# Performance work log

Hardware: AMD Instinct MI355X
Metric: run time of the kernel (lower is better)

Reference implementation:

```python
import jax, jax.numpy as jnp
import numpy as np

CHUNK = 128
KERNEL_EPS = 1e-4
ATTN_EPS = 1e-6


def _gaussian_orthogonal_random_matrix(nb_rows, nb_cols, seed=0):
    # scaling=0: rows of stacked orthogonal blocks, scaled by chi-distributed norms
    rng = np.random.default_rng(seed)
    blocks = []
    n_full = nb_rows // nb_cols
    for _ in range(n_full):
        qm, _ = np.linalg.qr(rng.standard_normal((nb_cols, nb_cols)))
        blocks.append(qm.T)
    rem = nb_rows - n_full * nb_cols
    if rem > 0:
        qm, _ = np.linalg.qr(rng.standard_normal((nb_cols, nb_cols)))
        blocks.append(qm.T[:rem])
    mat = np.concatenate(blocks, axis=0)
    multiplier = np.linalg.norm(rng.standard_normal((nb_rows, nb_cols)), axis=1)
    return (multiplier[:, None] * mat).astype(np.float32)


def softmax_kernel(data, proj, is_query):
    # data: [b,h,n,d], proj: [m,d]
    d = data.shape[-1]
    m = proj.shape[0]
    data_normalizer = d ** -0.25
    ratio = m ** -0.5
    data_dash = jnp.einsum('bhnd,md->bhnm', data * data_normalizer, proj)
    diag_data = (data ** 2).sum(-1, keepdims=True) * 0.5 * (data_normalizer ** 2)
    if is_query:
        stab = jnp.max(data_dash, axis=-1, keepdims=True)
    else:
        stab = jnp.max(data_dash)
    return ratio * (jnp.exp(data_dash - diag_data - stab) + KERNEL_EPS)


def chunked_causal_linear_attention(qf, kf, v):
    # qf,kf: [b,h,n,m]; v: [b,h,n,e]
    b, h, n, m = qf.shape
    e = v.shape[-1]
    nc = n // CHUNK
    to_chunks = lambda t: t.reshape(b, h, nc, CHUNK, -1).transpose(2, 0, 1, 3, 4)
    qc, kc, vc = to_chunks(qf), to_chunks(kf), to_chunks(v)  # [nc,b,h,c,*]

    def step(carry, xs):
        Z, S = carry  # Z: [b,h,m], S: [b,h,m,e]
        q, k, vv = xs
        k_cum = Z[:, :, None, :] + jnp.cumsum(k, axis=2)          # [b,h,c,m]
        D_inv = 1.0 / jnp.einsum('bhcm,bhcm->bhc', q, k_cum + ATTN_EPS)
        ctx = jnp.einsum('bhcm,bhce->bhcme', k, vv)               # [b,h,c,m,e]
        ctx_cum = S[:, :, None, :, :] + jnp.cumsum(ctx, axis=2)
        out = jnp.einsum('bhcme,bhcm,bhc->bhce', ctx_cum, q, D_inv)
        return (k_cum[:, :, -1, :], ctx_cum[:, :, -1, :, :]), out

    Z0 = jnp.zeros((b, h, m), qf.dtype)
    S0 = jnp.zeros((b, h, m, e), qf.dtype)
    (Z, S), outs = jax.lax.scan(jax.checkpoint(step), (Z0, S0), (qc, kc, vc))
    out = outs.transpose(1, 2, 0, 3, 4).reshape(b, h, n, e)
    return out, Z, S


def setup_inputs() -> dict:
    key = jax.random.key(0)
    kq, kk, kv = jax.random.split(key, 3)
    B, H, N, D, M = 2, 8, 4096, 64, 256
    q = jax.random.normal(kq, (B, H, N, D), dtype=jnp.float32)
    k = jax.random.normal(kk, (B, H, N, D), dtype=jnp.float32)
    v = jax.random.normal(kv, (B, H, N, D), dtype=jnp.float32)
    projection_matrix = jnp.asarray(_gaussian_orthogonal_random_matrix(M, D))
    return {"q": q, "k": k, "v": v, "projection_matrix": projection_matrix,
            "inferrring_states": 1}


def reference(q, k, v, projection_matrix, inferrring_states):
    qf = softmax_kernel(q, projection_matrix, is_query=True)
    kf = softmax_kernel(k, projection_matrix, is_query=False)
    out, Z, S = chunked_causal_linear_attention(qf, kf, v)
    return (out, Z, S)
```

## Files before the change

### kernel.cpp

```cpp
#include <hip/hip_runtime.h>

typedef unsigned short ushort_t;
typedef __attribute__((ext_vector_type(8))) short bf16x8;
typedef __attribute__((ext_vector_type(8))) _Float16 f16x8;
typedef __attribute__((ext_vector_type(16))) float f32x16;

#define NORMC 0.35355339059327373f
#define DIAGC 0.0625f
#define RATIO 0.0625f
#define KEPS  1e-4f
#define AEPS  1e-6f
#define KAPPA (RATIO*KEPS)

__device__ __forceinline__ unsigned short f2bf(float f){
  unsigned u = __float_as_uint(f);
  unsigned r = (u + 0x7FFFu + ((u >> 16) & 1u)) >> 16;
  return (unsigned short)r;
}
__device__ __forceinline__ float bf2f(unsigned short h){
  return __uint_as_float(((unsigned)h) << 16);
}
__device__ __forceinline__ unsigned enc_f(float f){
  unsigned u = __float_as_uint(f);
  return (u & 0x80000000u) ? ~u : (u | 0x80000000u);
}
__device__ __forceinline__ float dec_f(unsigned e){
  unsigned b = (e & 0x80000000u) ? (e ^ 0x80000000u) : ~e;
  return __uint_as_float(b);
}
__device__ __forceinline__ unsigned short h2u(_Float16 h){
  union { _Float16 h; unsigned short u; } c; c.h = h; return c.u;
}
__device__ __forceinline__ unsigned pk2h(float a, float b){
  return (unsigned)h2u((_Float16)a) | ((unsigned)h2u((_Float16)b) << 16);
}

__global__ void k_prep(const float* __restrict__ proj, ushort_t* __restrict__ pjh,
                       unsigned* __restrict__ kmax){
  int t = threadIdx.x;
  if (t == 0) *kmax = 0u;
  for (int d = 0; d < 64; ++d){
    float val = NORMC * proj[t*64 + d];
    pjh[t*64 + d] = h2u((_Float16)val);
  }
}

__launch_bounds__(512, 4)
__global__ void k_featQ(const float* __restrict__ q, const ushort_t* __restrict__ pjh,
                        ushort_t* __restrict__ qf)
{
  extern __shared__ char sm[];
  char* Bp = sm;
  char* Xh = sm + 32768;
  char* Xl = sm + 49152;
  float* dsm = (float*)(sm + 65536);
  float* rmx = (float*)(sm + 66048);

  int tid = threadIdx.x;
  int w   = tid >> 6;
  int wr  = w & 3;
  int wc  = w >> 2;
  int lane= tid & 63;
  int l31 = lane & 31;
  int half= lane >> 5;
  int tile = (int)blockIdx.x;
  int row0 = tile * 128;

  for (int i = tid; i < 2048; i += 512){
    int m = i >> 3, c8 = i & 7;
    int rgn = ((m>>5)*4 + (c8>>1))*2 + (c8&1);
    int slot = (m & 31) ^ ((rgn & 7) << 2);
    *(uint4*)(Bp + rgn*512 + slot*16) = *(const uint4*)(pjh + m*64 + c8*8);
  }
  #pragma unroll
  for (int it = 0; it < 4; ++it){
    int g = it*512 + tid;
    int row = g >> 4, c4 = g & 15;
    float4 xv = *(const float4*)(q + (size_t)(row0+row)*64 + c4*4);
    _Float16 h0=(_Float16)xv.x, h1=(_Float16)xv.y, h2=(_Float16)xv.z, h3=(_Float16)xv.w;
    float l0 = xv.x-(float)h0, l1 = xv.y-(float)h1, l2 = xv.z-(float)h2, l3 = xv.w-(float)h3;
    int rgn = ((row>>5)*4 + (c4>>2))*2 + ((c4>>1)&1);
    int off = rgn*512 + (((row&31) ^ ((c4>>1)<<2)))*16 + (c4&1)*8;
    uint2 ph; ph.x = (unsigned)h2u(h0)|((unsigned)h2u(h1)<<16);
              ph.y = (unsigned)h2u(h2)|((unsigned)h2u(h3)<<16);
    uint2 pl; pl.x = pk2h(l0,l1); pl.y = pk2h(l2,l3);
    *(uint2*)(Xh + off) = ph;
    *(uint2*)(Xl + off) = pl;
    float ssq = xv.x*xv.x + xv.y*xv.y + xv.z*xv.z + xv.w*xv.w;
    ssq += __shfl_xor(ssq, 1); ssq += __shfl_xor(ssq, 2);
    ssq += __shfl_xor(ssq, 4); ssq += __shfl_xor(ssq, 8);
    if ((tid & 15) == 0) dsm[row] = ssq;
  }
  __syncthreads();

  f16x8 ah[4], al[4];
  #pragma unroll
  for (int ks = 0; ks < 4; ++ks){
    int rgn = (wr*4+ks)*2+half;
    int off = rgn*512 + ((l31 ^ ((2*ks+half)<<2)))*16;
    ah[ks] = *(const f16x8*)(Xh + off);
    al[ks] = *(const f16x8*)(Xl + off);
  }
  f32x16 acc[4];
  #pragma unroll
  for (int ct=0; ct<4; ++ct){
    #pragma unroll
    for (int r=0; r<16; ++r) acc[ct][r] = 0.f;
  }
  #pragma unroll
  for (int ks = 0; ks < 4; ++ks){
    #pragma unroll
    for (int ct=0; ct<4; ++ct){
      int ctg = wc*4 + ct;
      int rgn = (ctg*4+ks)*2+half;
      f16x8 bv = *(const f16x8*)(Bp + rgn*512 + ((l31 ^ ((2*ks+half)<<2)))*16);
      acc[ct] = __builtin_amdgcn_mfma_f32_32x32x16_f16(ah[ks], bv, acc[ct], 0, 0, 0);
      acc[ct] = __builtin_amdgcn_mfma_f32_32x32x16_f16(al[ks], bv, acc[ct], 0, 0, 0);
    }
  }
  {
    float rmax[16];
    #pragma unroll
    for (int r=0; r<16; ++r){
      float mx = acc[0][r];
      #pragma unroll
      for (int ct=1; ct<4; ++ct) mx = fmaxf(mx, acc[ct][r]);
      #pragma unroll
      for (int s=1; s<32; s<<=1) mx = fmaxf(mx, __shfl_xor(mx, s));
      rmax[r] = mx;
    }
    if (l31 == 0){
      #pragma unroll
      for (int r=0; r<16; ++r)
        rmx[wc*128 + 32*wr + (r&3) + 8*(r>>2) + 4*half] = rmax[r];
    }
  }
  __syncthreads();

  float dgv[16], stv[16];
  #pragma unroll
  for (int r=0; r<16; ++r){
    int lrow = 32*wr + (r&3) + 8*(r>>2) + 4*half;
    dgv[r] = DIAGC * dsm[lrow];
    stv[r] = fmaxf(rmx[lrow], rmx[128+lrow]);
  }

  char* ob = sm;
  #pragma unroll
  for (int r=0; r<16; ++r){
    int lrow = 32*wr + (r&3) + 8*(r>>2) + 4*half;
    #pragma unroll
    for (int ct=0; ct<4; ++ct){
      int col = wc*128 + ct*32 + l31;
      float e = __expf(acc[ct][r] - dgv[r] - stv[r]);
      *(ushort_t*)(ob + lrow*512 + ((col*2) ^ ((lrow&15)<<4))) = f2bf(RATIO*(e + KEPS));
    }
  }
  __syncthreads();
  ushort_t* dst = qf + (size_t)row0*256;
  for (int i = tid; i < 4096; i += 512){
    int row = i >> 5, s = i & 31;
    uint4 d = *(const uint4*)(ob + row*512 + ((s*16) ^ ((row&15)<<4)));
    *(uint4*)(dst + (size_t)row*256 + ((s ^ (row&15)))*8) = d;
  }
}

__launch_bounds__(512, 2)
__global__ void k_chunkF(const float* __restrict__ kk, const float* __restrict__ v,
                         const ushort_t* __restrict__ pjh,
                         ushort_t* __restrict__ kfp, float* __restrict__ Zl,
                         float* __restrict__ Sl, float* __restrict__ vsb,
                         unsigned* __restrict__ kmax, float* __restrict__ lmArr)
{
  extern __shared__ char sm[];
  char* Bp = sm;
  char* Xh = sm + 32768;
  char* Xl = sm + 49152;
  char* ob = sm;
  char* kT = sm + 65536;
  char* vT = sm + 131072;
  float* dsm  = (float*)(sm + 147456);
  float* wred = (float*)(sm + 147968);

  int tid = threadIdx.x;
  int w   = tid >> 6;
  int wr  = w & 3;
  int wc  = w >> 2;
  int lane= tid & 63;
  int l31 = lane & 31;
  int half= lane >> 5;
  int cb  = (int)blockIdx.x;
  int bh  = cb >> 5, j = cb & 31;
  int row0 = bh*4096 + j*128;

  for (int i = tid; i < 2048; i += 512){
    int m = i >> 3, c8 = i & 7;
    int rgn = ((m>>5)*4 + (c8>>1))*2 + (c8&1);
    int slot = (m & 31) ^ ((rgn & 7) << 2);
    *(uint4*)(Bp + rgn*512 + slot*16) = *(const uint4*)(pjh + m*64 + c8*8);
  }
  #pragma unroll
  for (int it = 0; it < 4; ++it){
    int g = it*512 + tid;
    int row = g >> 4, c4 = g & 15;
    float4 xv = *(const float4*)(kk + (size_t)(row0+row)*64 + c4*4);
    _Float16 h0=(_Float16)xv.x, h1=(_Float16)xv.y, h2=(_Float16)xv.z, h3=(_Float16)xv.w;
    float l0 = xv.x-(float)h0, l1 = xv.y-(float)h1, l2 = xv.z-(float)h2, l3 = xv.w-(float)h3;
    int rgn = ((row>>5)*4 + (c4>>2))*2 + ((c4>>1)&1);
    int off = rgn*512 + (((row&31) ^ ((c4>>1)<<2)))*16 + (c4&1)*8;
    uint2 ph; ph.x = (unsigned)h2u(h0)|((unsigned)h2u(h1)<<16);
              ph.y = (unsigned)h2u(h2)|((unsigned)h2u(h3)<<16);
    uint2 pl; pl.x = pk2h(l0,l1); pl.y = pk2h(l2,l3);
    *(uint2*)(Xh + off) = ph;
    *(uint2*)(Xl + off) = pl;
    float ssq = xv.x*xv.x + xv.y*xv.y + xv.z*xv.z + xv.w*xv.w;
    ssq += __shfl_xor(ssq, 1); ssq += __shfl_xor(ssq, 2);
    ssq += __shfl_xor(ssq, 4); ssq += __shfl_xor(ssq, 8);
    if ((tid & 15) == 0) dsm[row] = ssq;
  }
  {
    int e = tid & 63, c0 = tid >> 6;
    int swz = (e & 15) << 4;
    #pragma unroll
    for (int u=0; u<16; ++u){
      int c = c0 + u*8;
      *(ushort_t*)(vT + e*256 + ((c*2) ^ swz)) = f2bf(v[(size_t)(row0+c)*64 + e]);
    }
  }
  __syncthreads();

  f16x8 ah[4], al[4];
  #pragma unroll
  for (int ks = 0; ks < 4; ++ks){
    int rgn = (wr*4+ks)*2+half;
    int off = rgn*512 + ((l31 ^ ((2*ks+half)<<2)))*16;
    ah[ks] = *(const f16x8*)(Xh + off);
    al[ks] = *(const f16x8*)(Xl + off);
  }
  f32x16 acc[4];
  #pragma unroll
  for (int ct=0; ct<4; ++ct){
    #pragma unroll
    for (int r=0; r<16; ++r) acc[ct][r] = 0.f;
  }
  #pragma unroll
  for (int ks = 0; ks < 4; ++ks){
    #pragma unroll
    for (int ct=0; ct<4; ++ct){
      int ctg = wc*4 + ct;
      int rgn = (ctg*4+ks)*2+half;
      f16x8 bv = *(const f16x8*)(Bp + rgn*512 + ((l31 ^ ((2*ks+half)<<2)))*16);
      acc[ct] = __builtin_amdgcn_mfma_f32_32x32x16_f16(ah[ks], bv, acc[ct], 0, 0, 0);
      acc[ct] = __builtin_amdgcn_mfma_f32_32x32x16_f16(al[ks], bv, acc[ct], 0, 0, 0);
    }
  }
  {
    float wm = acc[0][0];
    #pragma unroll
    for (int ct=0; ct<4; ++ct){
      #pragma unroll
      for (int r=0; r<16; ++r) wm = fmaxf(wm, acc[ct][r]);
    }
    #pragma unroll
    for (int s=1; s<32; s<<=1) wm = fmaxf(wm, __shfl_xor(wm, s));
    wm = fmaxf(wm, __shfl_xor(wm, 32));
    if (lane == 0) wred[w] = wm;
  }
  __syncthreads();
  float lmb = wred[0];
  #pragma unroll
  for (int i=1;i<8;++i) lmb = fmaxf(lmb, wred[i]);
  if (tid == 0){
    lmArr[cb] = lmb;
    atomicMax(kmax, enc_f(lmb));
  }
  float dgv[16];
  #pragma unroll
  for (int r=0; r<16; ++r)
    dgv[r] = DIAGC * dsm[32*wr + (r&3) + 8*(r>>2) + 4*half];

  #pragma unroll
  for (int ct=0; ct<4; ++ct){
    int m = wc*128 + ct*32 + l31;
    int swm = (m & 15) << 4;
    #pragma unroll
    for (int g=0; g<4; ++g){
      unsigned pk0=0, pk1=0;
      #pragma unroll
      for (int rr=0; rr<4; ++rr){
        int r = g*4 + rr;
        int c = 32*wr + rr + 8*g + 4*half;
        float e = __expf(acc[ct][r] - dgv[r] - lmb);
        unsigned b = f2bf(e);
        if (rr < 2) pk0 |= b << (16*rr); else pk1 |= b << (16*(rr-2));
        *(ushort_t*)(ob + c*512 + ((m*2) ^ ((c&15)<<4))) = (ushort_t)b;
      }
      int c0 = 32*wr + 8*g + 4*half;
      *(uint2*)(kT + m*256 + ((c0*2) ^ swm)) = make_uint2(pk0, pk1);
    }
  }
  __syncthreads();

  f32x16 accS[2], accz, avs[2];
  #pragma unroll
  for (int et=0;et<2;++et){
    #pragma unroll
    for (int r=0;r<16;++r){ accS[et][r]=0.f; avs[et][r]=0.f; }
  }
  #pragma unroll
  for (int r=0;r<16;++r) accz[r]=0.f;
  bf16x8 onesB, onesA;
  #pragma unroll
  for (int i=0;i<8;++i){
    onesB[i] = (l31==0) ? (short)0x3F80 : (short)0;
    onesA[i] = (short)0x3F80;
  }
  int erow = (w&1)*32 + l31;
  int mc0  = ((w>>1)*2 + 0)*32 + l31;
  int mc1  = ((w>>1)*2 + 1)*32 + l31;
  int mrow = 32*w + l31;
  #pragma unroll
  for (int ks=0; ks<8; ++ks){
    int koff = ks*32 + half*16;
    bf16x8 afv = *(const bf16x8*)(vT + erow*256 + (koff ^ ((erow&15)<<4)));
    bf16x8 bk0 = *(const bf16x8*)(kT + mc0*256 + (koff ^ ((mc0&15)<<4)));
    bf16x8 bk1 = *(const bf16x8*)(kT + mc1*256 + (koff ^ ((mc1&15)<<4)));
    bf16x8 afk = *(const bf16x8*)(kT + mrow*256 + (koff ^ ((mrow&15)<<4)));
    accS[0] = __builtin_amdgcn_mfma_f32_32x32x16_bf16(afv, bk0, accS[0], 0, 0, 0);
    accS[1] = __builtin_amdgcn_mfma_f32_32x32x16_bf16(afv, bk1, accS[1], 0, 0, 0);
    accz    = __builtin_amdgcn_mfma_f32_32x32x16_bf16(afk, onesB, accz, 0, 0, 0);
    if (w == 0){
      bf16x8 bv1 = *(const bf16x8*)(vT + (32+l31)*256 + (koff ^ (((32+l31)&15)<<4)));
      avs[0] = __builtin_amdgcn_mfma_f32_32x32x16_bf16(onesA, afv, avs[0], 0, 0, 0);
      avs[1] = __builtin_amdgcn_mfma_f32_32x32x16_bf16(onesA, bv1, avs[1], 0, 0, 0);
    }
  }
  #pragma unroll
  for (int r=0; r<16; ++r){
    int e = (w&1)*32 + (r&3) + 8*(r>>2) + 4*half;
    Sl[(size_t)cb*16384 + (size_t)e*256 + ((w>>1)*2+0)*32 + l31] = accS[0][r];
    Sl[(size_t)cb*16384 + (size_t)e*256 + ((w>>1)*2+1)*32 + l31] = accS[1][r];
  }
  if (l31 == 0){
    #pragma unroll
    for (int r=0; r<16; ++r){
      int m = 32*w + (r&3) + 8*(r>>2) + 4*half;
      Zl[(size_t)cb*256 + m] = accz[r];
    }
  }
  if (w == 0 && half == 0){
    vsb[(size_t)cb*64 + l31]      = avs[0][0];
    vsb[(size_t)cb*64 + 32 + l31] = avs[1][0];
  }
  {
    ushort_t* dst = kfp + (size_t)row0*256;
    for (int i = tid; i < 4096; i += 512){
      int row = i >> 5, s = i & 31;
      uint4 d = *(const uint4*)(ob + row*512 + ((s*16) ^ ((row&15)<<4)));
      *(uint4*)(dst + (size_t)row*256 + ((s ^ (row&15)))*8) = d;
    }
  }
}

__launch_bounds__(256)
__global__ void k_scan(float* __restrict__ Zl, const float* __restrict__ Sl,
                       const float* __restrict__ vsb, const float* __restrict__ lmArr,
                       const unsigned* __restrict__ kmax,
                       ushort_t* __restrict__ S0b,
                       float* __restrict__ outZ, float* __restrict__ outSt){
  float gm = dec_f(*kmax);
  int t = threadIdx.x;
  int bh = blockIdx.x / 65;
  int s  = blockIdx.x % 65;
  if (s == 64){
    size_t base = (size_t)(bh*32)*256 + t;
    float rz = 0.f;
    #pragma unroll
    for (int j0=0;j0<32;j0+=8){
      float x[8];
      #pragma unroll
      for (int u=0;u<8;++u){
        int cbx = bh*32 + j0 + u;
        float a = RATIO * __expf(lmArr[cbx] - gm);
        x[u] = fmaf(a, Zl[base + (size_t)(j0+u)*256], KAPPA*128.f);
      }
      #pragma unroll
      for (int u=0;u<8;++u){ Zl[base + (size_t)(j0+u)*256] = rz; rz += x[u]; }
    }
    outZ[(size_t)bh*256 + t] = rz;
  } else {
    size_t base = (size_t)(bh*32)*16384 + (size_t)s*256 + t;
    float rs = 0.f;
    #pragma unroll
    for (int j0=0;j0<32;j0+=8){
      float x[8];
      #pragma unroll
      for (int u=0;u<8;++u){
        int cbx = bh*32 + j0 + u;
        float a = RATIO * __expf(lmArr[cbx] - gm);
        x[u] = fmaf(a, Sl[base + (size_t)(j0+u)*16384], KAPPA * vsb[(size_t)cbx*64 + s]);
      }
      #pragma unroll
      for (int u=0;u<8;++u){
        S0b[(size_t)(bh*32 + j0+u)*16384 + (size_t)s*256 + t] = f2bf(rs);
        rs += x[u];
      }
    }
    outSt[(size_t)bh*16384 + (size_t)s*256 + t] = rs;
  }
}

__launch_bounds__(256)
__global__ void k_tr(const float* __restrict__ outSt, float* __restrict__ outS){
  __shared__ float tl[64][65];
  int tid = threadIdx.x;
  int bh = blockIdx.x >> 2, mt = blockIdx.x & 3;
  int m0 = mt*64;
  for (int i = tid; i < 4096; i += 256){
    int e = i >> 6, m = i & 63;
    tl[e][m] = outSt[(size_t)bh*16384 + (size_t)e*256 + m0 + m];
  }
  __syncthreads();
  for (int i = tid; i < 4096; i += 256){
    int m = i >> 6, e = i & 63;
    outS[(size_t)bh*16384 + (size_t)(m0+m)*64 + e] = tl[e][m];
  }
}

__launch_bounds__(512, 2)
__global__ void k_out(const ushort_t* __restrict__ qf, const ushort_t* __restrict__ kfp,
                      const float* __restrict__ v, const ushort_t* __restrict__ S0b,
                      const float* __restrict__ Zp, const float* __restrict__ lmArr,
                      const unsigned* __restrict__ kmax, float* __restrict__ outO)
{
  extern __shared__ char sm[];
  char* Ab   = sm;
  char* qft  = sm + 32768;
  char* vTb  = sm + 32768;
  char* ktb  = sm + 49152;
  char* s0t  = sm + 65536;
  float* rsc = (float*)(sm + 73728);
  ushort_t* z0b = (ushort_t*)(sm + 74752);

  int tid = threadIdx.x;
  int w   = tid >> 6;
  int wr  = w & 3;
  int wc  = w >> 2;
  int lane= tid & 63;
  int l31 = lane & 31;
  int half= lane >> 5;
  int pb  = (int)blockIdx.x;
  int bh  = pb >> 5, j = pb & 31;
  int row0 = bh*4096 + j*128;
  size_t qbase = (size_t)row0*256;

  float gmv = dec_f(*kmax);
  float alpha = RATIO * __expf(lmArr[pb] - gmv);

  if (tid < 256) z0b[tid] = f2bf(Zp[(size_t)pb*256 + tid] + AEPS);

  f32x16 accA[2], acc2, accQ;
  #pragma unroll
  for (int ct2=0;ct2<2;++ct2){
    #pragma unroll
    for (int r=0;r<16;++r) accA[ct2][r] = 0.f;
  }
  #pragma unroll
  for (int r=0;r<16;++r){ acc2[r] = 0.f; accQ[r] = 0.f; }

  int arow = 32*wr + l31;
  for (int mt=0; mt<4; ++mt){
    int m0 = mt*64;
    __syncthreads();
    #pragma unroll
    for (int u=0;u<2;++u){
      int ci = tid*2+u; int rr = ci>>3, c8 = ci&7;
      int dsw = (c8*16) ^ ((rr&7)<<4);
      *(uint4*)(qft + rr*128 + dsw) = *(const uint4*)(qf  + qbase + (size_t)rr*256 + m0 + c8*8);
      *(uint4*)(ktb + rr*128 + dsw) = *(const uint4*)(kfp + qbase + (size_t)rr*256 + m0 + c8*8);
    }
    {
      int e = tid >> 3, c8 = tid & 7;
      *(uint4*)(s0t + e*128 + ((c8*16) ^ ((e&7)<<4))) =
          *(const uint4*)(S0b + (size_t)pb*16384 + (size_t)e*256 + m0 + c8*8);
    }
    __syncthreads();
    #pragma unroll
    for (int ks=0;ks<4;++ks){
      int ko = ks*32 + half*16;
      bf16x8 af = *(const bf16x8*)(qft + arow*128 + (ko ^ ((arow&7)<<4)));
      {
        int er = wc*32 + l31;
        bf16x8 bS = *(const bf16x8*)(s0t + er*128 + (ko ^ ((er&7)<<4)));
        acc2 = __builtin_amdgcn_mfma_f32_32x32x16_bf16(af, bS, acc2, 0, 0, 0);
      }
      {
        bf16x8 zb = {};
        if (l31 == 0) zb = *(const bf16x8*)((const char*)z0b + m0*2 + ko);
        if (l31 == 1){
          #pragma unroll
          for (int i2=0;i2<8;++i2) zb[i2] = (short)0x3F80;
        }
        accQ = __builtin_amdgcn_mfma_f32_32x32x16_bf16(af, zb, accQ, 0, 0, 0);
      }
      #pragma unroll
      for (int ct2=0;ct2<2;++ct2){
        int c = wc*2 + ct2;
        if (c <= wr){
          int br = c*32 + l31;
          bf16x8 bk = *(const bf16x8*)(ktb + br*128 + (ko ^ ((br&7)<<4)));
          accA[ct2] = __builtin_amdgcn_mfma_f32_32x32x16_bf16(af, bk, accA[ct2], 0, 0, 0);
        }
      }
    }
  }

  float qzv[16], qfsv[16];
  #pragma unroll
  for (int r=0;r<16;++r){
    qzv[r]  = __shfl(accQ[r], half*32 + 0);
    qfsv[r] = __shfl(accQ[r], half*32 + 1);
  }

  {
    float p[16];
    #pragma unroll
    for (int r=0;r<16;++r) p[r]=0.f;
    #pragma unroll
    for (int ct2=0;ct2<2;++ct2){
      int c = wc*2 + ct2;
      if (c <= wr){
        #pragma unroll
        for (int r=0;r<16;++r){
          int grow = 32*wr + (r&3) + 8*(r>>2) + 4*half;
          int col  = c*32 + l31;
          float mval = (col <= grow) ? fmaf(alpha, accA[ct2][r], KAPPA*qfsv[r]) : 0.f;
          p[r] += mval;
          *(ushort_t*)(Ab + grow*256 + ((col*2) ^ ((grow&15)<<4))) = f2bf(mval);
        }
      }
    }
    #pragma unroll
    for (int s2=1;s2<32;s2<<=1){
      #pragma unroll
      for (int r=0;r<16;++r) p[r] += __shfl_xor(p[r], s2);
    }
    if (l31 == 0){
      #pragma unroll
      for (int r=0;r<16;++r)
        rsc[wc*128 + 32*wr + (r&3) + 8*(r>>2) + 4*half] = p[r];
    }
  }
  __syncthreads();

  {
    int e = tid & 63, c0 = tid >> 6;
    int swz = (e & 15) << 4;
    #pragma unroll
    for (int u=0; u<16; ++u){
      int c = c0 + u*8;
      *(ushort_t*)(vTb + e*256 + ((c*2) ^ swz)) = f2bf(v[(size_t)(row0+c)*64 + e]);
    }
  }
  __syncthreads();

  #pragma unroll
  for (int ks=0; ks<8; ++ks){
    if (ks <= 2*wr + 1){
      bf16x8 af = *(const bf16x8*)(Ab + arow*256 + ((ks*32 + half*16) ^ ((arow&15)<<4)));
      int er = wc*32 + l31;
      bf16x8 bv = *(const bf16x8*)(vTb + er*256 + ((ks*32 + half*16) ^ ((er&15)<<4)));
      acc2 = __builtin_amdgcn_mfma_f32_32x32x16_bf16(af, bv, acc2, 0, 0, 0);
    }
  }

  #pragma unroll
  for (int r=0;r<16;++r){
    int grow = 32*wr + (r&3) + 8*(r>>2) + 4*half;
    float dv = 1.0f / (rsc[grow] + rsc[128+grow] + qzv[r]);
    outO[(size_t)(row0+grow)*64 + wc*32 + l31] = acc2[r] * dv;
  }
}

extern "C" void kernel_launch(void* const* d_in, const int* in_sizes, int n_in,
                              void* d_out, int out_size, void* d_ws, size_t ws_size,
                              hipStream_t stream){
  (void)in_sizes; (void)n_in; (void)out_size; (void)ws_size;
  const float* q    = (const float*)d_in[0];
  const float* k    = (const float*)d_in[1];
  const float* v    = (const float*)d_in[2];
  const float* proj = (const float*)d_in[3];

  char* ws = (char*)d_ws;
  unsigned* kmax = (unsigned*)ws;
  float*    lmA  = (float*)(ws + 256);
  ushort_t* pjh  = (ushort_t*)(ws + 4096);
  ushort_t* kfp  = (ushort_t*)(ws + 65792);
  float*    Zl   = (float*)(ws + 33620224);
  float*    Sl   = (float*)(ws + 34144512);
  ushort_t* S0b  = (ushort_t*)(ws + 67698944);
  float*    vsb  = (float*)(ws + 84476160);
  float*    oSt  = (float*)(ws + 84607232);
  ushort_t* qfb  = (ushort_t*)(ws + 88801536);

  float* outO = (float*)d_out;
  float* outZ = outO + (size_t)2*8*4096*64;
  float* outS = outZ + 2*8*256;

  hipFuncSetAttribute((const void*)k_featQ,  hipFuncAttributeMaxDynamicSharedMemorySize, 67072);
  hipFuncSetAttribute((const void*)k_chunkF, hipFuncAttributeMaxDynamicSharedMemorySize, 148480);
  hipFuncSetAttribute((const void*)k_out,    hipFuncAttributeMaxDynamicSharedMemorySize, 75264);

  k_prep  <<<1,     256, 0, stream>>>(proj, pjh, kmax);
  k_featQ <<<512,   512, 67072, stream>>>(q, pjh, qfb);
  k_chunkF<<<512,   512, 148480, stream>>>(k, v, pjh, kfp, Zl, Sl, vsb, kmax, lmA);
  k_scan  <<<16*65, 256, 0, stream>>>(Zl, Sl, vsb, lmA, kmax, S0b, outZ, oSt);
  k_tr    <<<64,    256, 0, stream>>>(oSt, outS);
  k_out   <<<512,   512, 75264, stream>>>(qfb, kfp, v, S0b, Zl, lmA, kmax, outO);
}
```

Measured before the change: 108.9 us.

## Register-prefetch next q/k/S0 tiles and hoist V loads in output kernel

The m-tile loop now loads the next tile's qf, kf and S0 slices from global memory into registers while the MFMAs for the current tile run, so global latency overlaps compute instead of sitting between barriers. The V loads used later for the transposed V tile are issued at kernel start into 16 registers, hiding their latency behind the whole first phase. The cost is higher register pressure, which may lower occupancy or cause spills.

```diff
diff --git a/kernel.cpp b/kernel.cpp
--- a/kernel.cpp
+++ b/kernel.cpp
@@ -459,6 +459,28 @@
 
   if (tid < 256) z0b[tid] = f2bf(Zp[(size_t)pb*256 + tid] + AEPS);
 
+  int ve = tid & 63, vc0 = tid >> 6;
+  float vld[16];
+  #pragma unroll
+  for (int u=0; u<16; ++u)
+    vld[u] = v[(size_t)(row0 + vc0 + u*8)*64 + ve];
+
+  int rr0 = (tid*2)   >> 3, c80 = (tid*2)   & 7;
+  int rr1 = (tid*2+1) >> 3, c81 = (tid*2+1) & 7;
+  int se  = tid >> 3,  sc8 = tid & 7;
+  int dsw0 = (c80*16) ^ ((rr0&7)<<4);
+  int dsw1 = (c81*16) ^ ((rr1&7)<<4);
+  int dsws = (sc8*16) ^ ((se&7)<<4);
+
+  uint4 pq0, pq1, pk0v, pk1v, ps0v;
+  #define LOADT(m0_) do { \
+    pq0  = *(const uint4*)(qf  + qbase + (size_t)rr0*256 + (m0_) + c80*8); \
+    pq1  = *(const uint4*)(qf  + qbase + (size_t)rr1*256 + (m0_) + c81*8); \
+    pk0v = *(const uint4*)(kfp + qbase + (size_t)rr0*256 + (m0_) + c80*8); \
+    pk1v = *(const uint4*)(kfp + qbase + (size_t)rr1*256 + (m0_) + c81*8); \
+    ps0v = *(const uint4*)(S0b + (size_t)pb*16384 + (size_t)se*256 + (m0_) + sc8*8); \
+  } while(0)
+
   f32x16 accA[2], acc2, accQ;
   #pragma unroll
   for (int ct2=0;ct2<2;++ct2){
@@ -469,22 +491,19 @@
   for (int r=0;r<16;++r){ acc2[r] = 0.f; accQ[r] = 0.f; }
 
   int arow = 32*wr + l31;
+  LOADT(0);
+
+  #pragma unroll
   for (int mt=0; mt<4; ++mt){
     int m0 = mt*64;
     __syncthreads();
-    #pragma unroll
-    for (int u=0;u<2;++u){
-      int ci = tid*2+u; int rr = ci>>3, c8 = ci&7;
-      int dsw = (c8*16) ^ ((rr&7)<<4);
-      *(uint4*)(qft + rr*128 + dsw) = *(const uint4*)(qf  + qbase + (size_t)rr*256 + m0 + c8*8);
-      *(uint4*)(ktb + rr*128 + dsw) = *(const uint4*)(kfp + qbase + (size_t)rr*256 + m0 + c8*8);
-    }
-    {
-      int e = tid >> 3, c8 = tid & 7;
-      *(uint4*)(s0t + e*128 + ((c8*16) ^ ((e&7)<<4))) =
-          *(const uint4*)(S0b + (size_t)pb*16384 + (size_t)e*256 + m0 + c8*8);
-    }
+    *(uint4*)(qft + rr0*128 + dsw0) = pq0;
+    *(uint4*)(qft + rr1*128 + dsw1) = pq1;
+    *(uint4*)(ktb + rr0*128 + dsw0) = pk0v;
+    *(uint4*)(ktb + rr1*128 + dsw1) = pk1v;
+    *(uint4*)(s0t + se*128  + dsws) = ps0v;
     __syncthreads();
+    if (mt < 3) LOADT((mt+1)*64);
     #pragma unroll
     for (int ks=0;ks<4;++ks){
       int ko = ks*32 + half*16;
@@ -514,6 +533,7 @@
       }
     }
   }
+  #undef LOADT
 
   float qzv[16], qfsv[16];
   #pragma unroll
@@ -554,12 +574,11 @@
   __syncthreads();
 
   {
-    int e = tid & 63, c0 = tid >> 6;
-    int swz = (e & 15) << 4;
+    int swz = (ve & 15) << 4;
     #pragma unroll
     for (int u=0; u<16; ++u){
-      int c = c0 + u*8;
-      *(ushort_t*)(vTb + e*256 + ((c*2) ^ swz)) = f2bf(v[(size_t)(row0+c)*64 + e]);
+      int c = vc0 + u*8;
+      *(ushort_t*)(vTb + ve*256 + ((c*2) ^ swz)) = f2bf(vld[u]);
     }
   }
   __syncthreads();
```

Measured after the change: 106.8 us. -2.0%, faster.
